# Kernel optimization log

Measured on AMD Instinct MI355X. Metric: run time of the kernel, lower is better.

The kernel has to match this reference:

```python
import jax, jax.numpy as jnp
import numpy as np

D = 256   # embedding dim d; rows are d+1 = 257
N = 2048  # sequence length n; cols are n+1 = 2049
B = 16

def setup_inputs() -> dict:
    key = jax.random.key(0)
    k_h, k_p, k_q = jax.random.split(key, 3)
    H = jax.random.normal(k_h, (B, D + 1, N + 1), dtype=jnp.float32)
    P = jax.random.normal(k_p, (D + 1, D + 1), dtype=jnp.float32) * 0.01
    Q = jax.random.normal(k_q, (D + 1, D + 1), dtype=jnp.float32) * 0.01
    return {"H": H, "P": P, "Q": Q}

def reference(H, P, Q):
    # H: (B, d+1, n+1)
    n = H.shape[2] - 1
    # HtQH = H^T @ Q @ H : (B, n+1, n+1)
    HtQ = jnp.einsum('bds,de->bse', H, Q)          # (B, n+1, d+1)
    HtQH = jnp.einsum('bse,bet->bst', HtQ, H)      # (B, n+1, n+1)
    # mask M = diag(1,...,1,0): M @ HtQH zeroes the last row
    MHtQH = HtQH.at[:, -1, :].set(0.0)
    PH = jnp.einsum('de,bet->bdt', P, H)           # (B, d+1, n+1)
    attn = jnp.einsum('bds,bst->bdt', PH, MHtQH)   # (B, d+1, n+1)
    return H + attn / n
```

## Files before the change

kernel.cpp:

```cpp
#include <hip/hip_runtime.h>
#include <hip/hip_bf16.h>

#define DP     257
#define NP     2049
#define NSEQ   2048
#define NB     16
#define KLD    288
#define HROWS  320
#define TPITCH 320
#define TROWS  2176
#define KPAD   40

typedef __attribute__((ext_vector_type(8))) short bf16x8;
typedef __attribute__((ext_vector_type(4))) short bf16x4;
typedef __attribute__((ext_vector_type(4))) float f32x4;

__global__ __launch_bounds__(256) void conv_all(const float* __restrict__ H,
                                                const float* __restrict__ P,
                                                const float* __restrict__ Q,
                                                __hip_bfloat16* __restrict__ Hb,
                                                __hip_bfloat16* __restrict__ Hbt,
                                                __hip_bfloat16* __restrict__ Pb,
                                                __hip_bfloat16* __restrict__ Qt) {
    const int z  = blockIdx.z;
    const int tl = threadIdx.x & 63;
    const int er = threadIdx.x >> 6;
    __shared__ float tile[64][65];

    if (z < NB) {
        const int b  = z;
        const int t0 = blockIdx.x * 64;
        const int e0 = blockIdx.y * 64;
        const float* __restrict__ Hs = H + (size_t)b * DP * NP;
        __hip_bfloat16* __restrict__ Hbb  = Hb  + (size_t)b * HROWS * 2048;
        __hip_bfloat16* __restrict__ Hbtb = Hbt + (size_t)b * TROWS * TPITCH;

#pragma unroll
        for (int r = 0; r < 16; ++r) {
            const int el = er + r * 4;
            const int ge = e0 + el;
            const int gt = t0 + tl;
            float v = 0.f;
            if (ge < DP && gt < NP) v = Hs[(size_t)ge * NP + gt];
            tile[el][tl] = v;
            if (ge < HROWS && gt < 2048) Hbb[(size_t)ge * 2048 + gt] = __float2bfloat16(v);
        }
        __syncthreads();
#pragma unroll
        for (int r = 0; r < 16; ++r) {
            const int ttl = er + r * 4;
            const int gt = t0 + ttl;
            const int ge = e0 + tl;
            if (gt < TROWS && ge < TPITCH) {
                const float v = (ge < KLD) ? tile[tl][ttl] : 0.f;
                Hbtb[(size_t)gt * TPITCH + ge] = __float2bfloat16(v);
            }
        }
        return;
    }

    const int bx = blockIdx.x;
    if (bx >= 10) return;
    const int r0 = blockIdx.y * 64;
    if (bx < 5) {
        const int c0 = bx * 64;
#pragma unroll
        for (int r = 0; r < 16; ++r) {
            const int m = r0 + er + r * 4;
            const int k = c0 + tl;
            float v = (m < DP && k < DP) ? P[m * DP + k] : 0.f;
            if (m < KLD && k < KLD) Pb[m * KLD + k] = __float2bfloat16(v);
        }
    } else {
        const int c0 = (bx - 5) * 64;
#pragma unroll
        for (int r = 0; r < 16; ++r) {
            const int k = r0 + er + r * 4;
            const int n = c0 + tl;
            float v = (k < DP && n < DP) ? Q[k * DP + n] : 0.f;
            tile[k - r0][n - c0] = v;
        }
        __syncthreads();
#pragma unroll
        for (int r = 0; r < 16; ++r) {
            const int k = r0 + tl;
            const int n = c0 + er + r * 4;
            if (n < KLD && k < KLD) Qt[n * KLD + k] = __float2bfloat16(tile[tl][n - c0]);
        }
    }
}

__global__ __launch_bounds__(512, 4) void gram_staged(const __hip_bfloat16* __restrict__ Hb,
                                                      __hip_bfloat16* __restrict__ G) {
    const int b  = blockIdx.y;
    const int tm = blockIdx.x / 5;
    const int tn = blockIdx.x % 5;
    const int m0 = tm * 64, n0 = tn * 64;
    const int tid = threadIdx.x;
    const int wave = tid >> 6, lane = tid & 63;
    const int lrow = lane & 15, kq = (lane >> 4) * 8;
    const int hw = wave >> 2;
    const int q  = wave & 3;
    const int mh = (q & 1) * 32, nh = (q >> 1) * 32;
    const int hs = tid >> 8;
    const int t2 = tid & 255;
    const int sr = t2 >> 2;
    const int sc = (t2 & 3) * 8;

    __shared__ __align__(16) char smem[2 * 2 * 2 * 64 * KPAD * 2];
    short* As = (short*)smem;
    short* Bs = (short*)(smem + 2 * 2 * 64 * KPAD * 2);
    float* red = (float*)smem;

    const short* __restrict__ base = (const short*)(Hb + (size_t)b * HROWS * 2048);

    auto aoff = [&](int buf, int h, int r) { return ((buf * 2 + h) * 64 + r) * KPAD; };

    f32x4 acc[2][2] = {};

    {
        const int kb = hs * 1024;
        *(bf16x8*)&As[aoff(0, hs, sr) + sc] = *(const bf16x8*)(base + (size_t)(m0 + sr) * 2048 + kb + sc);
        *(bf16x8*)&Bs[aoff(0, hs, sr) + sc] = *(const bf16x8*)(base + (size_t)(n0 + sr) * 2048 + kb + sc);
    }
    __syncthreads();

    for (int kt = 0; kt < 32; ++kt) {
        const int cur = kt & 1, nxt = cur ^ 1;
        if (kt + 1 < 32) {
            const int kb = hs * 1024 + (kt + 1) * 32;
            *(bf16x8*)&As[aoff(nxt, hs, sr) + sc] = *(const bf16x8*)(base + (size_t)(m0 + sr) * 2048 + kb + sc);
            *(bf16x8*)&Bs[aoff(nxt, hs, sr) + sc] = *(const bf16x8*)(base + (size_t)(n0 + sr) * 2048 + kb + sc);
        }
        bf16x8 a0 = *(const bf16x8*)&As[aoff(cur, hw, mh + lrow) + kq];
        bf16x8 a1 = *(const bf16x8*)&As[aoff(cur, hw, mh + 16 + lrow) + kq];
        bf16x8 b0 = *(const bf16x8*)&Bs[aoff(cur, hw, nh + lrow) + kq];
        bf16x8 b1 = *(const bf16x8*)&Bs[aoff(cur, hw, nh + 16 + lrow) + kq];
        acc[0][0] = __builtin_amdgcn_mfma_f32_16x16x32_bf16(a0, b0, acc[0][0], 0, 0, 0);
        acc[0][1] = __builtin_amdgcn_mfma_f32_16x16x32_bf16(a0, b1, acc[0][1], 0, 0, 0);
        acc[1][0] = __builtin_amdgcn_mfma_f32_16x16x32_bf16(a1, b0, acc[1][0], 0, 0, 0);
        acc[1][1] = __builtin_amdgcn_mfma_f32_16x16x32_bf16(a1, b1, acc[1][1], 0, 0, 0);
        __syncthreads();
    }

    const int ccol  = lane & 15;
    const int crow0 = (lane >> 4) * 4;
#pragma unroll
    for (int i = 0; i < 2; ++i)
#pragma unroll
        for (int j = 0; j < 2; ++j)
#pragma unroll
            for (int r = 0; r < 4; ++r)
                red[((wave * 32) + i * 16 + crow0 + r) * 32 + j * 16 + ccol] = acc[i][j][r];
    __syncthreads();

    const int q2  = tid >> 7;
    const int t7  = tid & 127;
    const int row = t7 >> 2;
    const int c8  = (t7 & 3) * 8;
    const int gm = m0 + (q2 & 1) * 32 + row;
    const int gn = n0 + (q2 >> 1) * 32 + c8;
    if (gm < KLD && gn < KLD) {
        __hip_bfloat16 o[8];
#pragma unroll
        for (int t = 0; t < 8; ++t) {
            const float v = red[((q2 * 32) + row) * 32 + c8 + t] +
                            red[(((q2 + 4) * 32) + row) * 32 + c8 + t];
            o[t] = __float2bfloat16((gm < DP && (gn + t) < DP) ? v : 0.f);
        }
        __hip_bfloat16* __restrict__ Gb = G + (size_t)b * KLD * KLD;
        *(bf16x8*)&Gb[gm * KLD + gn] = *(const bf16x8*)o;
    }
}

__global__ __launch_bounds__(256) void mm_sk4(const __hip_bfloat16* __restrict__ A,
                                              const __hip_bfloat16* __restrict__ B,
                                              __hip_bfloat16* __restrict__ C,
                                              int strideA, int strideB) {
    const int b  = blockIdx.y;
    const int tm = blockIdx.x / 9;
    const int tn = blockIdx.x % 9;
    const int s    = threadIdx.x >> 6;
    const int lane = threadIdx.x & 63;
    const int lrow = lane & 15;
    const int koff = (lane >> 4) * 8;
    const short* __restrict__ Ab = (const short*)(A + (size_t)b * strideA);
    const short* __restrict__ Bb = (const short*)(B + (size_t)b * strideB);
    const int m0 = tm * 32, n0 = tn * 32;

    __shared__ float red[4][32][32];

    f32x4 acc[2][2] = {};
    for (int kt = s; kt < 9; kt += 4) {
        const int k0 = kt * 32;
        bf16x8 a0 = *(const bf16x8*)(Ab + (m0 + lrow)      * KLD + k0 + koff);
        bf16x8 a1 = *(const bf16x8*)(Ab + (m0 + 16 + lrow) * KLD + k0 + koff);
        bf16x8 c0 = *(const bf16x8*)(Bb + (n0 + lrow)      * KLD + k0 + koff);
        bf16x8 c1 = *(const bf16x8*)(Bb + (n0 + 16 + lrow) * KLD + k0 + koff);
        acc[0][0] = __builtin_amdgcn_mfma_f32_16x16x32_bf16(a0, c0, acc[0][0], 0, 0, 0);
        acc[0][1] = __builtin_amdgcn_mfma_f32_16x16x32_bf16(a0, c1, acc[0][1], 0, 0, 0);
        acc[1][0] = __builtin_amdgcn_mfma_f32_16x16x32_bf16(a1, c0, acc[1][0], 0, 0, 0);
        acc[1][1] = __builtin_amdgcn_mfma_f32_16x16x32_bf16(a1, c1, acc[1][1], 0, 0, 0);
    }

    const int ccol  = lane & 15;
    const int crow0 = (lane >> 4) * 4;
#pragma unroll
    for (int i = 0; i < 2; ++i)
#pragma unroll
        for (int j = 0; j < 2; ++j)
#pragma unroll
            for (int r = 0; r < 4; ++r)
                red[s][i * 16 + crow0 + r][j * 16 + ccol] = acc[i][j][r];
    __syncthreads();

    const int row = threadIdx.x >> 3;
    const int c4  = (threadIdx.x & 7) * 4;
    float4 v0 = *(const float4*)&red[0][row][c4];
    float4 v1 = *(const float4*)&red[1][row][c4];
    float4 v2 = *(const float4*)&red[2][row][c4];
    float4 v3 = *(const float4*)&red[3][row][c4];
    float sum[4] = {v0.x + v1.x + v2.x + v3.x,
                    v0.y + v1.y + v2.y + v3.y,
                    v0.z + v1.z + v2.z + v3.z,
                    v0.w + v1.w + v2.w + v3.w};
    const int gm = m0 + row;
    const int gn = n0 + c4;
    __hip_bfloat16 o[4];
#pragma unroll
    for (int t = 0; t < 4; ++t) {
        const float v = (gm < DP && (gn + t) < DP) ? sum[t] : 0.f;
        o[t] = __float2bfloat16(v);
    }
    __hip_bfloat16* __restrict__ Cb = C + (size_t)b * KLD * KLD;
    *(bf16x4*)&Cb[gm * KLD + gn] = *(const bf16x4*)o;
}

__global__ __launch_bounds__(256, 4) void attn_v6(const __hip_bfloat16* __restrict__ Kb,
                                                  const __hip_bfloat16* __restrict__ Hbt,
                                                  const float* __restrict__ H,
                                                  float* __restrict__ Out) {
    const int id      = blockIdx.x;
    const int logical = (id & 7) * 170 + (id >> 3);
    const int b   = logical / 85;
    const int rem = logical % 85;
    const int t0  = (rem / 5) * 128;
    const int d0  = (rem % 5) * 64;

    const int tid = threadIdx.x;
    const int wave = tid >> 6, lane = tid & 63;
    const int lrow = lane & 15, kq = (lane >> 4) * 8;
    const int dh = (wave & 1) * 32;
    const int th = (wave >> 1) * 64;
    const int sr = tid >> 2;
    const int sc = (tid & 3) * 8;

    __shared__ __align__(16) char smem[2 * (64 + 128) * KPAD * 2];
    short* bufs = (short*)smem;
    float* Ped  = (float*)smem;

    const short* __restrict__ Ka = (const short*)(Kb  + (size_t)b * KLD * KLD);
    const short* __restrict__ Ta = (const short*)(Hbt + (size_t)b * TROWS * TPITCH);

    int rA = d0 + sr; if (rA > KLD - 1) rA = KLD - 1;
    const short* __restrict__ gA  = Ka + (size_t)rA * KLD + sc;
    const short* __restrict__ gB0 = Ta + (size_t)(t0 + sr) * TPITCH + sc;
    const short* __restrict__ gB1 = Ta + (size_t)(t0 + 64 + sr) * TPITCH + sc;

    auto Aoff = [&](int bi, int r) { return (bi * 192 + r) * KPAD; };
    auto Boff = [&](int bi, int r) { return (bi * 192 + 64 + r) * KPAD; };

    f32x4 acc[2][4] = {};

    {
        bf16x8 a = *(const bf16x8*)gA;
        bf16x8 x = *(const bf16x8*)gB0;
        bf16x8 y = *(const bf16x8*)gB1;
        *(bf16x8*)&bufs[Aoff(0, sr) + sc]      = a;
        *(bf16x8*)&bufs[Boff(0, sr) + sc]      = x;
        *(bf16x8*)&bufs[Boff(0, 64 + sr) + sc] = y;
    }
    bf16x8 rA1 = *(const bf16x8*)(gA  + 32);
    bf16x8 rB0 = *(const bf16x8*)(gB0 + 32);
    bf16x8 rB1 = *(const bf16x8*)(gB1 + 32);
    __syncthreads();

#pragma unroll
    for (int kt = 0; kt < 9; ++kt) {
        const int cur = kt & 1;
        bf16x8 nA, nB0, nB1;
        if (kt < 7) {
            const int e = (kt + 2) * 32;
            nA  = *(const bf16x8*)(gA  + e);
            nB0 = *(const bf16x8*)(gB0 + e);
            nB1 = *(const bf16x8*)(gB1 + e);
        }
        bf16x8 af0 = *(const bf16x8*)&bufs[Aoff(cur, dh + lrow) + kq];
        bf16x8 af1 = *(const bf16x8*)&bufs[Aoff(cur, dh + 16 + lrow) + kq];
        bf16x8 bfr[4];
#pragma unroll
        for (int j = 0; j < 4; ++j)
            bfr[j] = *(const bf16x8*)&bufs[Boff(cur, th + j * 16 + lrow) + kq];
#pragma unroll
        for (int j = 0; j < 4; ++j) {
            acc[0][j] = __builtin_amdgcn_mfma_f32_16x16x32_bf16(af0, bfr[j], acc[0][j], 0, 0, 0);
            acc[1][j] = __builtin_amdgcn_mfma_f32_16x16x32_bf16(af1, bfr[j], acc[1][j], 0, 0, 0);
        }
        if (kt < 8) {
            *(bf16x8*)&bufs[Aoff(cur ^ 1, sr) + sc]      = rA1;
            *(bf16x8*)&bufs[Boff(cur ^ 1, sr) + sc]      = rB0;
            *(bf16x8*)&bufs[Boff(cur ^ 1, 64 + sr) + sc] = rB1;
        }
        __syncthreads();
        if (kt < 7) { rA1 = nA; rB0 = nB0; rB1 = nB1; }
    }

    const float* __restrict__ Hs = H + (size_t)b * DP * NP;
    float* __restrict__ Ob = Out + (size_t)b * DP * NP;
    const float inv_n = 1.0f / (float)NSEQ;
    const int ccol  = lane & 15;
    const int crow0 = (lane >> 4) * 4;
    const int prow = tid >> 5;
    const int pcol = (tid & 31) * 4;

    float hreg[4][2][4];
#pragma unroll
    for (int c = 0; c < 4; ++c)
#pragma unroll
        for (int p = 0; p < 2; ++p) {
            const int gd = d0 + c * 16 + p * 8 + prow;
            if (gd < DP) {
                const size_t base = (size_t)gd * NP + t0;
#pragma unroll
                for (int cc = 0; cc < 4; ++cc) {
                    const int gt = t0 + pcol + cc;
                    if (gt < NP) hreg[c][p][cc] = Hs[base + pcol + cc];
                }
            }
        }

#pragma unroll
    for (int c2 = 0; c2 < 2; ++c2) {
        if ((wave & 1) == c2) {
#pragma unroll
            for (int i = 0; i < 2; ++i)
#pragma unroll
                for (int j = 0; j < 4; ++j)
#pragma unroll
                    for (int r = 0; r < 4; ++r)
                        Ped[(i * 16 + crow0 + r) * 132 + th + j * 16 + ccol] = acc[i][j][r];
        }
        __syncthreads();
#pragma unroll
        for (int c = 2 * c2; c < 2 * c2 + 2; ++c)
#pragma unroll
            for (int p = 0; p < 2; ++p) {
                const int rloc = (c & 1) * 16 + p * 8 + prow;
                const int gd = d0 + c * 16 + p * 8 + prow;
                if (gd < DP) {
                    const float4 pv = *(const float4*)&Ped[rloc * 132 + pcol];
                    const size_t base = (size_t)gd * NP + t0;
                    const float pva[4] = {pv.x, pv.y, pv.z, pv.w};
#pragma unroll
                    for (int cc = 0; cc < 4; ++cc) {
                        const int gt = t0 + pcol + cc;
                        if (gt < NP) Ob[base + pcol + cc] = hreg[c][p][cc] + inv_n * pva[cc];
                    }
                }
            }
        if (c2 == 0) __syncthreads();
    }
}

extern "C" void kernel_launch(void* const* d_in, const int* in_sizes, int n_in,
                              void* d_out, int out_size, void* d_ws, size_t ws_size,
                              hipStream_t stream) {
    const float* H = (const float*)d_in[0];
    const float* P = (const float*)d_in[1];
    const float* Q = (const float*)d_in[2];
    float* out = (float*)d_out;

    __hip_bfloat16* Hb  = (__hip_bfloat16*)d_ws;
    __hip_bfloat16* Hbt = Hb  + (size_t)NB * HROWS * 2048;
    __hip_bfloat16* G   = Hbt + (size_t)NB * TROWS * TPITCH;
    __hip_bfloat16* Pb  = G   + (size_t)NB * KLD * KLD;
    __hip_bfloat16* Qt  = Pb  + (size_t)KLD * KLD;
    __hip_bfloat16* W   = Hb;
    __hip_bfloat16* Kb  = Hb + (size_t)NB * KLD * KLD;

    conv_all<<<dim3(34, 5, NB + 1), 256, 0, stream>>>(H, P, Q, Hb, Hbt, Pb, Qt);
    gram_staged<<<dim3(25, NB), 512, 0, stream>>>(Hb, G);
    mm_sk4<<<dim3(81, NB), 256, 0, stream>>>(Pb, G, W, 0, KLD * KLD);
    mm_sk4<<<dim3(81, NB), 256, 0, stream>>>(W, Qt, Kb, KLD * KLD, 0);
    attn_v6<<<dim3(17 * 5 * NB), 256, 0, stream>>>(Kb, Hbt, H, out);
}
```

Before: 173.6 us.

## Exploit Gram symmetry and drop padded final K-tile in attention GEMM

```diff
diff --git a/kernel.cpp b/kernel.cpp
--- a/kernel.cpp
+++ b/kernel.cpp
@@ -93,8 +93,9 @@
 __global__ __launch_bounds__(512, 4) void gram_staged(const __hip_bfloat16* __restrict__ Hb,
                                                       __hip_bfloat16* __restrict__ G) {
     const int b  = blockIdx.y;
-    const int tm = blockIdx.x / 5;
-    const int tn = blockIdx.x % 5;
+    int idx = blockIdx.x, tm = 0, w = 5;
+    while (idx >= w) { idx -= w; ++tm; --w; }
+    const int tn = tm + idx;
     const int m0 = tm * 64, n0 = tn * 64;
     const int tid = threadIdx.x;
     const int wave = tid >> 6, lane = tid & 63;
@@ -158,18 +159,36 @@
     const int t7  = tid & 127;
     const int row = t7 >> 2;
     const int c8  = (t7 & 3) * 8;
-    const int gm = m0 + (q2 & 1) * 32 + row;
-    const int gn = n0 + (q2 >> 1) * 32 + c8;
-    if (gm < KLD && gn < KLD) {
-        __hip_bfloat16 o[8];
-#pragma unroll
-        for (int t = 0; t < 8; ++t) {
-            const float v = red[((q2 * 32) + row) * 32 + c8 + t] +
-                            red[(((q2 + 4) * 32) + row) * 32 + c8 + t];
-            o[t] = __float2bfloat16((gm < DP && (gn + t) < DP) ? v : 0.f);
-        }
-        __hip_bfloat16* __restrict__ Gb = G + (size_t)b * KLD * KLD;
-        *(bf16x8*)&Gb[gm * KLD + gn] = *(const bf16x8*)o;
+    __hip_bfloat16* __restrict__ Gb = G + (size_t)b * KLD * KLD;
+
+    {
+        const int gm = m0 + (q2 & 1) * 32 + row;
+        const int gn = n0 + (q2 >> 1) * 32 + c8;
+        if (gm < KLD && gn < KLD) {
+            __hip_bfloat16 o[8];
+#pragma unroll
+            for (int t = 0; t < 8; ++t) {
+                const float v = red[((q2 * 32) + row) * 32 + c8 + t] +
+                                red[(((q2 + 4) * 32) + row) * 32 + c8 + t];
+                o[t] = __float2bfloat16((gm < DP && (gn + t) < DP) ? v : 0.f);
+            }
+            *(bf16x8*)&Gb[gm * KLD + gn] = *(const bf16x8*)o;
+        }
+    }
+    if (tm != tn) {
+        const int gm = n0 + (q2 & 1) * 32 + row;
+        const int gn = m0 + (q2 >> 1) * 32 + c8;
+        if (gm < KLD && gn < KLD) {
+            const int qp = ((q2 >> 1) & 1) | ((q2 & 1) << 1);
+            __hip_bfloat16 o[8];
+#pragma unroll
+            for (int t = 0; t < 8; ++t) {
+                const float v = red[((qp * 32) + c8 + t) * 32 + row] +
+                                red[(((qp + 4) * 32) + c8 + t) * 32 + row];
+                o[t] = __float2bfloat16((gm < DP && (gn + t) < DP) ? v : 0.f);
+            }
+            *(bf16x8*)&Gb[gm * KLD + gn] = *(const bf16x8*)o;
+        }
     }
 }
 
@@ -236,7 +255,7 @@
     *(bf16x4*)&Cb[gm * KLD + gn] = *(const bf16x4*)o;
 }
 
-__global__ __launch_bounds__(256, 4) void attn_v6(const __hip_bfloat16* __restrict__ Kb,
+__global__ __launch_bounds__(256, 4) void attn_v7(const __hip_bfloat16* __restrict__ Kb,
                                                   const __hip_bfloat16* __restrict__ Hbt,
                                                   const float* __restrict__ H,
                                                   float* __restrict__ Out) {
@@ -254,6 +273,8 @@
     const int th = (wave >> 1) * 64;
     const int sr = tid >> 2;
     const int sc = (tid & 3) * 8;
+    const int ccol  = lane & 15;
+    const int crow0 = (lane >> 4) * 4;
 
     __shared__ __align__(16) char smem[2 * (64 + 128) * KPAD * 2];
     short* bufs = (short*)smem;
@@ -286,10 +307,10 @@
     __syncthreads();
 
 #pragma unroll
-    for (int kt = 0; kt < 9; ++kt) {
+    for (int kt = 0; kt < 8; ++kt) {
         const int cur = kt & 1;
         bf16x8 nA, nB0, nB1;
-        if (kt < 7) {
+        if (kt < 6) {
             const int e = (kt + 2) * 32;
             nA  = *(const bf16x8*)(gA  + e);
             nB0 = *(const bf16x8*)(gB0 + e);
@@ -306,20 +327,38 @@
             acc[0][j] = __builtin_amdgcn_mfma_f32_16x16x32_bf16(af0, bfr[j], acc[0][j], 0, 0, 0);
             acc[1][j] = __builtin_amdgcn_mfma_f32_16x16x32_bf16(af1, bfr[j], acc[1][j], 0, 0, 0);
         }
-        if (kt < 8) {
+        if (kt < 7) {
             *(bf16x8*)&bufs[Aoff(cur ^ 1, sr) + sc]      = rA1;
             *(bf16x8*)&bufs[Boff(cur ^ 1, sr) + sc]      = rB0;
             *(bf16x8*)&bufs[Boff(cur ^ 1, 64 + sr) + sc] = rB1;
         }
         __syncthreads();
-        if (kt < 7) { rA1 = nA; rB0 = nB0; rB1 = nB1; }
+        if (kt < 6) { rA1 = nA; rB0 = nB0; rB1 = nB1; }
+    }
+
+    {
+        float bv[4];
+#pragma unroll
+        for (int j = 0; j < 4; ++j) {
+            const int tt = t0 + th + j * 16 + ccol;
+            bv[j] = __bfloat162float(*(const __hip_bfloat16*)&Ta[(size_t)tt * TPITCH + 256]);
+        }
+#pragma unroll
+        for (int i = 0; i < 2; ++i)
+#pragma unroll
+            for (int r = 0; r < 4; ++r) {
+                int rr = d0 + dh + i * 16 + crow0 + r;
+                if (rr > KLD - 1) rr = KLD - 1;
+                const float av = __bfloat162float(*(const __hip_bfloat16*)&Ka[(size_t)rr * KLD + 256]);
+#pragma unroll
+                for (int j = 0; j < 4; ++j)
+                    acc[i][j][r] += av * bv[j];
+            }
     }
 
     const float* __restrict__ Hs = H + (size_t)b * DP * NP;
     float* __restrict__ Ob = Out + (size_t)b * DP * NP;
     const float inv_n = 1.0f / (float)NSEQ;
-    const int ccol  = lane & 15;
-    const int crow0 = (lane >> 4) * 4;
     const int prow = tid >> 5;
     const int pcol = (tid & 31) * 4;
 
@@ -389,8 +428,8 @@
     __hip_bfloat16* Kb  = Hb + (size_t)NB * KLD * KLD;
 
     conv_all<<<dim3(34, 5, NB + 1), 256, 0, stream>>>(H, P, Q, Hb, Hbt, Pb, Qt);
-    gram_staged<<<dim3(25, NB), 512, 0, stream>>>(Hb, G);
+    gram_staged<<<dim3(15, NB), 512, 0, stream>>>(Hb, G);
     mm_sk4<<<dim3(81, NB), 256, 0, stream>>>(Pb, G, W, 0, KLD * KLD);
     mm_sk4<<<dim3(81, NB), 256, 0, stream>>>(W, Qt, Kb, KLD * KLD, 0);
-    attn_v6<<<dim3(17 * 5 * NB), 256, 0, stream>>>(Kb, Hbt, H, out);
+    attn_v7<<<dim3(17 * 5 * NB), 256, 0, stream>>>(Kb, Hbt, H, out);
 }
```

New measurement: 166.6 us. 4.1% less time.
